# Kernel tuning notes

Measured on AMD Instinct MI355X. Metric: run time of the kernel, lower is better.

## Reference

```python
import jax, jax.numpy as jnp
import numpy as np

B = 32768          # batch
NA = 8             # n_agents
A = NA - 1         # other agents
OBS = 64
ACT = 14
OTH_IN = 82        # (sum(obs)+sum(act)-obs_i+act_i)//(NA-1)
H_SELF = 64
H_OTH = 128
H2 = 64
HEADS = 4
AD = H_OTH // HEADS  # 32
MAX_ACTION = 1.0
SCALE = float(np.sqrt(AD))


def setup_inputs() -> dict:
    key = jax.random.key(0)
    ks = jax.random.split(key, 24)
    r = jax.random.normal
    u = jax.random.uniform
    inp = {
        "state_one": r(ks[0], (B, OBS), jnp.float32),
        "act_one": u(ks[1], (B, ACT), jnp.float32),
        "state_others": r(ks[2], (A, B, OBS), jnp.float32),
        "act_others": u(ks[3], (A, B, OTH_IN - OBS), jnp.float32),
        # self encoder
        "W1": r(ks[4], (OBS + ACT, H_SELF), jnp.float32) * 0.05,
        "b1": r(ks[5], (H_SELF,), jnp.float32) * 0.05,
        "W2": r(ks[6], (H_SELF, H_SELF), jnp.float32) * 0.05,
        "b2": r(ks[7], (H_SELF,), jnp.float32) * 0.05,
        "w3_self": r(ks[8], (H_SELF, H2), jnp.float32) * 0.01,  # init.normal_(0, 0.01)
        # per-other-agent encoders (stacked ModuleList)
        "We": r(ks[9], (A, OTH_IN, H_OTH), jnp.float32) * 0.05,
        "be": r(ks[10], (A, H_OTH), jnp.float32) * 0.05,
        # attention heads (stacked)
        "Wk": r(ks[11], (HEADS, H_OTH, AD), jnp.float32) * 0.05,   # no bias
        "Wq": r(ks[12], (HEADS, H_SELF, AD), jnp.float32) * 0.05,  # no bias
        "Wv": r(ks[13], (HEADS, H_OTH, AD), jnp.float32) * 0.05,
        "bv": r(ks[14], (HEADS, AD), jnp.float32) * 0.05,
        "w3_others": r(ks[15], (H_OTH, H2), jnp.float32) * 0.01,
        "Wout": r(ks[16], (H2, 1), jnp.float32) * 0.05,
        "bout": r(ks[17], (1,), jnp.float32) * 0.05,
    }
    return inp


def reference(state_one, act_one, state_others, act_others,
              W1, b1, W2, b2, w3_self, We, be,
              Wk, Wq, Wv, bv, w3_others, Wout, bout):
    act_one = act_one / MAX_ACTION
    act_others = act_others / MAX_ACTION

    # self branch
    x = jnp.concatenate([state_one, act_one], axis=-1)          # [B, 78]
    x1 = jax.nn.relu(x @ W1 + b1)                               # [B, 64]
    x2 = jax.nn.relu(x1 @ W2 + b2)                              # [B, 64]
    x3_self = x2 @ w3_self                                      # [B, 64]

    # per-other-agent encoders
    inps = jnp.concatenate([state_others, act_others], axis=-1)  # [A, B, 82]
    enc = jax.nn.relu(jnp.einsum('abi,aij->abj', inps, We) + be[:, None, :])  # [A, B, 128]

    # multi-head attention: query from x1 (self), keys/values from encodings
    keys = jnp.einsum('abj,hjd->habd', enc, Wk)                  # [H, A, B, d]
    vals = jax.nn.relu(jnp.einsum('abj,hjd->habd', enc, Wv) + bv[:, None, None, :])
    sel = jnp.einsum('bj,hjd->hbd', x1, Wq)                      # [H, B, d]
    logits = jnp.einsum('hbd,habd->hba', sel, keys) / SCALE      # [H, B, A]
    w = jax.nn.softmax(logits, axis=-1)
    ov = jnp.einsum('habd,hba->hbd', vals, w)                    # [H, B, d]

    # concat heads along feature dim (head-major, as torch.cat over head list)
    x2_others = jnp.transpose(ov, (1, 0, 2)).reshape(-1, HEADS * AD)  # [B, 128]
    x3_others = x2_others @ w3_others                            # [B, 64]

    x3 = jax.nn.relu(x3_self + x3_others)
    return x3 @ Wout + bout                                      # [B, 1]
```

## Files before the change

kernel.cpp:

```cpp
#include <hip/hip_runtime.h>
#include <hip/hip_bf16.h>

#define BTOT 32768
#define TB 32

typedef __attribute__((ext_vector_type(8))) short bhalf8;
typedef __attribute__((ext_vector_type(4))) float f32x4;

static __device__ __forceinline__ unsigned short f2bf(float x) {
    __hip_bfloat16 h = __float2bfloat16(x);
    unsigned short u;
    __builtin_memcpy(&u, &h, sizeof(u));
    return u;
}
static __device__ __forceinline__ float bf2f(unsigned short s) {
    return __uint_as_float(((unsigned int)s) << 16);
}

__global__ __launch_bounds__(256) void prep_all(
        const float* __restrict__ Wk, const float* __restrict__ Wq,
        const float* __restrict__ We, const float* __restrict__ Wv,
        const float* __restrict__ W2, const float* __restrict__ w3_self,
        const float* __restrict__ w3_others, const float* __restrict__ W1,
        unsigned short* __restrict__ Mf2, unsigned short* __restrict__ Wef2,
        unsigned short* __restrict__ Wvf2, unsigned short* __restrict__ W2f,
        unsigned short* __restrict__ w3sf, unsigned short* __restrict__ w3of,
        unsigned short* __restrict__ W1f)
{
    const int blk = blockIdx.x;
    if (blk < 128) {
        int tid = blk * 256 + threadIdx.x;
        int h  = tid >> 13;
        int jq = (tid >> 7) & 63;
        int j  = tid & 127;
        const float* q = Wq + (h*64 + jq)*32;
        const float* k = Wk + (h*128 + j)*32;
        float acc = 0.f;
#pragma unroll
        for (int d = 0; d < 32; d += 4) {
            float4 a = *(const float4*)(q + d);
            float4 b = *(const float4*)(k + d);
            acc += a.x*b.x + a.y*b.y + a.z*b.z + a.w*b.w;
        }
        unsigned short hi = f2bf(acc);
        unsigned short lo = f2bf(acc - bf2f(hi));
        int n  = h*128 + j;
        int kt = jq >> 5, qd = (jq >> 3) & 3, jj = jq & 7;
        int nt = n >> 4,  ln = n & 15;
        size_t base = (((nt*2 + kt)*64) + qd*16 + ln)*16;
        Mf2[base + jj]     = hi;
        Mf2[base + 8 + jj] = lo;
    } else if (blk < 464) {
        int tid = (blk - 128) * 256 + threadIdx.x;
        int a = tid / 12288;
        int r = tid - a*12288;
        int k = r >> 7;
        int n = r & 127;
        float v = (k < 82) ? We[((size_t)a*82 + k)*128 + n] : 0.f;
        unsigned short hi = f2bf(v);
        unsigned short lo = f2bf(v - bf2f(hi));
        int kt = k >> 5, qd = (k >> 3) & 3, j = k & 7;
        int nt = n >> 4, ln = n & 15;
        size_t base = (size_t)a*24576 + (((nt*3 + kt)*64) + qd*16 + ln)*16;
        Wef2[base + j]     = hi;
        Wef2[base + 8 + j] = lo;
    } else if (blk < 528) {
        int tid = (blk - 464) * 256 + threadIdx.x;
        int h = tid >> 12;
        int j = (tid >> 5) & 127;
        int d = tid & 31;
        float v = Wv[tid];
        unsigned short hi = f2bf(v);
        unsigned short lo = f2bf(v - bf2f(hi));
        int k = j, n = h*32 + d;
        int kt = k >> 5, qd = (k >> 3) & 3, jj = k & 7;
        int nt = n >> 4, ln = n & 15;
        size_t base = (((nt*4 + kt)*64) + qd*16 + ln)*16;
        Wvf2[base + jj]     = hi;
        Wvf2[base + 8 + jj] = lo;
    } else {
        int tid = (blk - 528) * 256 + threadIdx.x;
        const float* src;
        unsigned short* dst;
        int idx, KT, kmax;
        if (tid < 4096)       { src = W2;        dst = W2f;  idx = tid;         KT = 2; kmax = 64; }
        else if (tid < 8192)  { src = w3_self;   dst = w3sf; idx = tid - 4096;  KT = 2; kmax = 64; }
        else if (tid < 16384) { src = w3_others; dst = w3of; idx = tid - 8192;  KT = 4; kmax = 128; }
        else                  { src = W1;        dst = W1f;  idx = tid - 16384; KT = 3; kmax = 78; }
        int k = idx >> 6;
        int n = idx & 63;
        float v = (k < kmax) ? src[k*64 + n] : 0.f;
        unsigned short hi = f2bf(v);
        unsigned short lo = f2bf(v - bf2f(hi));
        int kt = k >> 5, qd = (k >> 3) & 3, j = k & 7;
        int nt = n >> 4, ln = n & 15;
        size_t base = (((nt*KT + kt)*64) + qd*16 + ln)*16;
        dst[base + j]     = hi;
        dst[base + 8 + j] = lo;
    }
}

__global__ __launch_bounds__(256, 2) void fused_critic(
    const float* __restrict__ state_one, const float* __restrict__ act_one,
    const float* __restrict__ state_others, const float* __restrict__ act_others,
    const float* __restrict__ b1, const float* __restrict__ b2,
    const float* __restrict__ be, const float* __restrict__ bvp,
    const float* __restrict__ Wout, const float* __restrict__ bout,
    const unsigned short* __restrict__ Mf2, const unsigned short* __restrict__ Wef2,
    const unsigned short* __restrict__ Wvf2, const unsigned short* __restrict__ W2f,
    const unsigned short* __restrict__ w3sf, const unsigned short* __restrict__ w3of,
    const unsigned short* __restrict__ W1f, float* __restrict__ out)
{
    __shared__ __align__(16) unsigned char smem[33280];
    unsigned short* sXbH  = (unsigned short*)smem;
    unsigned short* sXbL  = (unsigned short*)(smem + 6656);
    unsigned short* sX1bH = (unsigned short*)(smem + 13312);
    unsigned short* sX1bL = (unsigned short*)(smem + 17920);
    unsigned short* sX2bH = (unsigned short*)(smem + 22528);
    unsigned short* sX2bL = (unsigned short*)(smem + 27136);
    unsigned short* sT    = (unsigned short*)smem;
    unsigned short* sInH  = (unsigned short*)smem;
    unsigned short* sInL  = (unsigned short*)(smem + 6656);
    unsigned short* sEnH  = (unsigned short*)(smem + 13312);
    unsigned short* sEnL  = (unsigned short*)(smem + 22016);
    unsigned short* sOvH  = (unsigned short*)smem;
    unsigned short* sOvL  = (unsigned short*)(smem + 8704);
    float*          sRed  = (float*)(smem + 17408);

    const int t  = threadIdx.x;
    const int b0 = blockIdx.x * TB;
    const int w  = t >> 6;
    const int l  = t & 63;
    const int m  = l & 15;
    const int qd = l >> 4;

    const int act_r = t >> 3, act_c = t & 7;

    auto stageIn = [&](const float4& vA, const float4& vB, const float* av) {
        const int r0 = t >> 4, c4 = (t & 15) << 2;
        ushort4 h4, l4;
        h4.x = f2bf(vA.x); l4.x = f2bf(vA.x - bf2f(h4.x));
        h4.y = f2bf(vA.y); l4.y = f2bf(vA.y - bf2f(h4.y));
        h4.z = f2bf(vA.z); l4.z = f2bf(vA.z - bf2f(h4.z));
        h4.w = f2bf(vA.w); l4.w = f2bf(vA.w - bf2f(h4.w));
        *(ushort4*)(sInH + r0*104 + c4) = h4;
        *(ushort4*)(sInL + r0*104 + c4) = l4;
        h4.x = f2bf(vB.x); l4.x = f2bf(vB.x - bf2f(h4.x));
        h4.y = f2bf(vB.y); l4.y = f2bf(vB.y - bf2f(h4.y));
        h4.z = f2bf(vB.z); l4.z = f2bf(vB.z - bf2f(h4.z));
        h4.w = f2bf(vB.w); l4.w = f2bf(vB.w - bf2f(h4.w));
        *(ushort4*)(sInH + (r0+16)*104 + c4) = h4;
        *(ushort4*)(sInL + (r0+16)*104 + c4) = l4;
        if (act_c < 6) {
#pragma unroll
            for (int e = 0; e < 3; ++e) {
                float v = av[e];
                unsigned short hh = f2bf(v);
                sInH[act_r*104 + 64 + act_c*3 + e] = hh;
                sInL[act_r*104 + 64 + act_c*3 + e] = f2bf(v - bf2f(hh));
            }
        }
    };

    {
        const int r0 = t >> 4, c4 = (t & 15) << 2;
        float4 vA = *(const float4*)(state_one + (size_t)(b0 + r0)*64 + c4);
        float4 vB = *(const float4*)(state_one + (size_t)(b0 + r0 + 16)*64 + c4);
        ushort4 h4, l4;
        h4.x = f2bf(vA.x); l4.x = f2bf(vA.x - bf2f(h4.x));
        h4.y = f2bf(vA.y); l4.y = f2bf(vA.y - bf2f(h4.y));
        h4.z = f2bf(vA.z); l4.z = f2bf(vA.z - bf2f(h4.z));
        h4.w = f2bf(vA.w); l4.w = f2bf(vA.w - bf2f(h4.w));
        *(ushort4*)(sXbH + r0*104 + c4) = h4;
        *(ushort4*)(sXbL + r0*104 + c4) = l4;
        h4.x = f2bf(vB.x); l4.x = f2bf(vB.x - bf2f(h4.x));
        h4.y = f2bf(vB.y); l4.y = f2bf(vB.y - bf2f(h4.y));
        h4.z = f2bf(vB.z); l4.z = f2bf(vB.z - bf2f(h4.z));
        h4.w = f2bf(vB.w); l4.w = f2bf(vB.w - bf2f(h4.w));
        *(ushort4*)(sXbH + (r0+16)*104 + c4) = h4;
        *(ushort4*)(sXbL + (r0+16)*104 + c4) = l4;
#pragma unroll
        for (int e = 0; e < 2; ++e) {
            int cc = act_c*2 + e;
            float v = (cc < 14) ? act_one[(size_t)(b0 + act_r)*14 + cc] : 0.f;
            unsigned short hh = f2bf(v);
            sXbH[act_r*104 + 64 + cc] = hh;
            sXbL[act_r*104 + 64 + cc] = f2bf(v - bf2f(hh));
        }
        for (int f = t; f < TB*16; f += 256) {
            int r = f >> 4, c = 80 + (f & 15);
            sXbH[r*104 + c] = 0;
            sXbL[r*104 + c] = 0;
        }
    }
    __syncthreads();

    {
        f32x4 acc1[2] = {};
#pragma unroll
        for (int kt = 0; kt < 3; ++kt) {
            bhalf8 ah0 = *(const bhalf8*)(sXbH + m*104      + kt*32 + qd*8);
            bhalf8 ah1 = *(const bhalf8*)(sXbH + (16+m)*104 + kt*32 + qd*8);
            bhalf8 al0 = *(const bhalf8*)(sXbL + m*104      + kt*32 + qd*8);
            bhalf8 al1 = *(const bhalf8*)(sXbL + (16+m)*104 + kt*32 + qd*8);
            const unsigned short* bp = W1f + ((w*3 + kt)*64 + l)*16;
            bhalf8 bh = *(const bhalf8*)(bp);
            bhalf8 bl = *(const bhalf8*)(bp + 8);
            acc1[0] = __builtin_amdgcn_mfma_f32_16x16x32_bf16(ah0, bh, acc1[0], 0, 0, 0);
            acc1[1] = __builtin_amdgcn_mfma_f32_16x16x32_bf16(ah1, bh, acc1[1], 0, 0, 0);
            acc1[0] = __builtin_amdgcn_mfma_f32_16x16x32_bf16(ah0, bl, acc1[0], 0, 0, 0);
            acc1[1] = __builtin_amdgcn_mfma_f32_16x16x32_bf16(ah1, bl, acc1[1], 0, 0, 0);
            acc1[0] = __builtin_amdgcn_mfma_f32_16x16x32_bf16(al0, bh, acc1[0], 0, 0, 0);
            acc1[1] = __builtin_amdgcn_mfma_f32_16x16x32_bf16(al1, bh, acc1[1], 0, 0, 0);
        }
        int col = w*16 + m;
        float b1c = b1[col];
#pragma unroll
        for (int rt = 0; rt < 2; ++rt)
#pragma unroll
            for (int r = 0; r < 4; ++r) {
                float e = fmaxf(acc1[rt][r] + b1c, 0.f);
                int row = rt*16 + qd*4 + r;
                unsigned short hh = f2bf(e);
                sX1bH[row*72 + col] = hh;
                sX1bL[row*72 + col] = f2bf(e - bf2f(hh));
            }
    }
    __syncthreads();

    {
        f32x4 acc2[2] = {};
#pragma unroll
        for (int kt = 0; kt < 2; ++kt) {
            bhalf8 ah0 = *(const bhalf8*)(sX1bH + m*72      + kt*32 + qd*8);
            bhalf8 ah1 = *(const bhalf8*)(sX1bH + (16+m)*72 + kt*32 + qd*8);
            bhalf8 al0 = *(const bhalf8*)(sX1bL + m*72      + kt*32 + qd*8);
            bhalf8 al1 = *(const bhalf8*)(sX1bL + (16+m)*72 + kt*32 + qd*8);
            const unsigned short* bp = W2f + ((w*2 + kt)*64 + l)*16;
            bhalf8 bh = *(const bhalf8*)(bp);
            bhalf8 bl = *(const bhalf8*)(bp + 8);
            acc2[0] = __builtin_amdgcn_mfma_f32_16x16x32_bf16(ah0, bh, acc2[0], 0, 0, 0);
            acc2[1] = __builtin_amdgcn_mfma_f32_16x16x32_bf16(ah1, bh, acc2[1], 0, 0, 0);
            acc2[0] = __builtin_amdgcn_mfma_f32_16x16x32_bf16(ah0, bl, acc2[0], 0, 0, 0);
            acc2[1] = __builtin_amdgcn_mfma_f32_16x16x32_bf16(ah1, bl, acc2[1], 0, 0, 0);
            acc2[0] = __builtin_amdgcn_mfma_f32_16x16x32_bf16(al0, bh, acc2[0], 0, 0, 0);
            acc2[1] = __builtin_amdgcn_mfma_f32_16x16x32_bf16(al1, bh, acc2[1], 0, 0, 0);
        }
        int col = w*16 + m;
        float b2c = b2[col];
#pragma unroll
        for (int rt = 0; rt < 2; ++rt)
#pragma unroll
            for (int r = 0; r < 4; ++r) {
                float e = fmaxf(acc2[rt][r] + b2c, 0.f);
                int row = rt*16 + qd*4 + r;
                unsigned short hh = f2bf(e);
                sX2bH[row*72 + col] = hh;
                sX2bL[row*72 + col] = f2bf(e - bf2f(hh));
            }
    }
    __syncthreads();

    f32x4 x3a[2] = {};
    {
#pragma unroll
        for (int kt = 0; kt < 2; ++kt) {
            bhalf8 ah0 = *(const bhalf8*)(sX2bH + m*72      + kt*32 + qd*8);
            bhalf8 ah1 = *(const bhalf8*)(sX2bH + (16+m)*72 + kt*32 + qd*8);
            bhalf8 al0 = *(const bhalf8*)(sX2bL + m*72      + kt*32 + qd*8);
            bhalf8 al1 = *(const bhalf8*)(sX2bL + (16+m)*72 + kt*32 + qd*8);
            const unsigned short* bp = w3sf + ((w*2 + kt)*64 + l)*16;
            bhalf8 bh = *(const bhalf8*)(bp);
            bhalf8 bl = *(const bhalf8*)(bp + 8);
            x3a[0] = __builtin_amdgcn_mfma_f32_16x16x32_bf16(ah0, bh, x3a[0], 0, 0, 0);
            x3a[1] = __builtin_amdgcn_mfma_f32_16x16x32_bf16(ah1, bh, x3a[1], 0, 0, 0);
            x3a[0] = __builtin_amdgcn_mfma_f32_16x16x32_bf16(ah0, bl, x3a[0], 0, 0, 0);
            x3a[1] = __builtin_amdgcn_mfma_f32_16x16x32_bf16(ah1, bl, x3a[1], 0, 0, 0);
            x3a[0] = __builtin_amdgcn_mfma_f32_16x16x32_bf16(al0, bh, x3a[0], 0, 0, 0);
            x3a[1] = __builtin_amdgcn_mfma_f32_16x16x32_bf16(al1, bh, x3a[1], 0, 0, 0);
        }
    }

    {
        f32x4 tacc[2][8] = {};
#pragma unroll
        for (int kt = 0; kt < 2; ++kt) {
            bhalf8 ah0 = *(const bhalf8*)(sX1bH + m*72      + kt*32 + qd*8);
            bhalf8 ah1 = *(const bhalf8*)(sX1bH + (16+m)*72 + kt*32 + qd*8);
            bhalf8 al0 = *(const bhalf8*)(sX1bL + m*72      + kt*32 + qd*8);
            bhalf8 al1 = *(const bhalf8*)(sX1bL + (16+m)*72 + kt*32 + qd*8);
#pragma unroll
            for (int nt2 = 0; nt2 < 8; ++nt2) {
                int nt = w*8 + nt2;
                const unsigned short* bp = Mf2 + ((nt*2 + kt)*64 + l)*16;
                bhalf8 bh = *(const bhalf8*)(bp);
                bhalf8 bl = *(const bhalf8*)(bp + 8);
                tacc[0][nt2] = __builtin_amdgcn_mfma_f32_16x16x32_bf16(ah0, bh, tacc[0][nt2], 0, 0, 0);
                tacc[1][nt2] = __builtin_amdgcn_mfma_f32_16x16x32_bf16(ah1, bh, tacc[1][nt2], 0, 0, 0);
                tacc[0][nt2] = __builtin_amdgcn_mfma_f32_16x16x32_bf16(ah0, bl, tacc[0][nt2], 0, 0, 0);
                tacc[1][nt2] = __builtin_amdgcn_mfma_f32_16x16x32_bf16(ah1, bl, tacc[1][nt2], 0, 0, 0);
                tacc[0][nt2] = __builtin_amdgcn_mfma_f32_16x16x32_bf16(al0, bh, tacc[0][nt2], 0, 0, 0);
                tacc[1][nt2] = __builtin_amdgcn_mfma_f32_16x16x32_bf16(al1, bh, tacc[1][nt2], 0, 0, 0);
            }
        }
        __syncthreads();
#pragma unroll
        for (int rt = 0; rt < 2; ++rt)
#pragma unroll
            for (int nt2 = 0; nt2 < 8; ++nt2)
#pragma unroll
                for (int r = 0; r < 4; ++r)
                    sT[(rt*16 + qd*4 + r)*520 + w*128 + nt2*16 + m] =
                        f2bf(tacc[rt][nt2][r]);
    }
    __syncthreads();

    bhalf8 tB0[4], tB1[4];
    {
#pragma unroll
        for (int kt = 0; kt < 4; ++kt) {
            tB0[kt] = *(const bhalf8*)(sT + m*520      + w*128 + kt*32 + qd*8);
            tB1[kt] = *(const bhalf8*)(sT + (16+m)*520 + w*128 + kt*32 + qd*8);
        }
    }
    __syncthreads();

    for (int f = t; f < TB*16; f += 256) {
        int r = f >> 4, c = f & 15;
        if (c >= 2) {
            sInH[r*104 + 80 + c] = 0;
            sInL[r*104 + 80 + c] = 0;
        }
    }
    {
        const float* sa = state_others + (size_t)b0 * 64;
        float4 vA = *(const float4*)(sa + t*4);
        float4 vB = *(const float4*)(sa + t*4 + 1024);
        float av[3] = {0.f, 0.f, 0.f};
        if (act_c < 6) {
            const float* aa = act_others + (size_t)(b0 + act_r)*18 + act_c*3;
            av[0] = aa[0]; av[1] = aa[1]; av[2] = aa[2];
        }
        stageIn(vA, vB, av);
    }
    __syncthreads();

    const float bv0 = bvp[w*32 + m];
    const float bv1 = bvp[w*32 + 16 + m];
    f32x4 o4[2][2] = {};
    float mR = -1e30f, sR = 0.f;

    const int nsel = l & 15;
    const int srcl = ((nsel >> 2) << 4) | nsel;

    float4 pfA, pfB; float pfa[3] = {0.f, 0.f, 0.f};

    for (int a = 0; a < 7; ++a) {
        if (a < 6) {
            const float* sa = state_others + ((size_t)(a+1)*BTOT + b0)*64;
            pfA = *(const float4*)(sa + t*4);
            pfB = *(const float4*)(sa + t*4 + 1024);
            if (act_c < 6) {
                const float* aa = act_others
                    + ((size_t)(a+1)*BTOT + b0 + act_r)*18 + act_c*3;
                pfa[0] = aa[0]; pfa[1] = aa[1]; pfa[2] = aa[2];
            }
        }
        float be0 = be[a*128 + 32*w + m];
        float be1 = be[a*128 + 32*w + 16 + m];

        f32x4 eacc[2][2] = {};
#pragma unroll
        for (int kt = 0; kt < 3; ++kt) {
            bhalf8 ah0 = *(const bhalf8*)(sInH + m*104      + kt*32 + qd*8);
            bhalf8 ah1 = *(const bhalf8*)(sInH + (16+m)*104 + kt*32 + qd*8);
            bhalf8 al0 = *(const bhalf8*)(sInL + m*104      + kt*32 + qd*8);
            bhalf8 al1 = *(const bhalf8*)(sInL + (16+m)*104 + kt*32 + qd*8);
#pragma unroll
            for (int nt2 = 0; nt2 < 2; ++nt2) {
                int nt = 2*w + nt2;
                const unsigned short* bp =
                    Wef2 + (size_t)a*24576 + ((nt*3 + kt)*64 + l)*16;
                bhalf8 bh = *(const bhalf8*)(bp);
                bhalf8 bl = *(const bhalf8*)(bp + 8);
                eacc[0][nt2] = __builtin_amdgcn_mfma_f32_16x16x32_bf16(ah0, bh, eacc[0][nt2], 0, 0, 0);
                eacc[1][nt2] = __builtin_amdgcn_mfma_f32_16x16x32_bf16(ah1, bh, eacc[1][nt2], 0, 0, 0);
                eacc[0][nt2] = __builtin_amdgcn_mfma_f32_16x16x32_bf16(ah0, bl, eacc[0][nt2], 0, 0, 0);
                eacc[1][nt2] = __builtin_amdgcn_mfma_f32_16x16x32_bf16(ah1, bl, eacc[1][nt2], 0, 0, 0);
                eacc[0][nt2] = __builtin_amdgcn_mfma_f32_16x16x32_bf16(al0, bh, eacc[0][nt2], 0, 0, 0);
                eacc[1][nt2] = __builtin_amdgcn_mfma_f32_16x16x32_bf16(al1, bh, eacc[1][nt2], 0, 0, 0);
            }
        }

        __syncthreads();

        {
#pragma unroll
            for (int rt = 0; rt < 2; ++rt)
#pragma unroll
                for (int nt2 = 0; nt2 < 2; ++nt2) {
                    float bb = nt2 ? be1 : be0;
#pragma unroll
                    for (int r = 0; r < 4; ++r) {
                        float e = fmaxf(eacc[rt][nt2][r] + bb, 0.f);
                        int row = rt*16 + qd*4 + r;
                        int col = 32*w + nt2*16 + m;
                        unsigned short hh = f2bf(e);
                        sEnH[row*136 + col] = hh;
                        sEnL[row*136 + col] = f2bf(e - bf2f(hh));
                    }
                }
        }
        if (a < 6) stageIn(pfA, pfB, pfa);

        __syncthreads();

        f32x4 vacc[2][2] = {};
        f32x4 lacc0 = {}, lacc1 = {};
#pragma unroll
        for (int kt = 0; kt < 4; ++kt) {
            bhalf8 ah0 = *(const bhalf8*)(sEnH + m*136      + kt*32 + qd*8);
            bhalf8 ah1 = *(const bhalf8*)(sEnH + (16+m)*136 + kt*32 + qd*8);
            bhalf8 al0 = *(const bhalf8*)(sEnL + m*136      + kt*32 + qd*8);
            bhalf8 al1 = *(const bhalf8*)(sEnL + (16+m)*136 + kt*32 + qd*8);
#pragma unroll
            for (int nt2 = 0; nt2 < 2; ++nt2) {
                int nt = 2*w + nt2;
                const unsigned short* bp = Wvf2 + ((nt*4 + kt)*64 + l)*16;
                bhalf8 bh = *(const bhalf8*)(bp);
                bhalf8 bl = *(const bhalf8*)(bp + 8);
                vacc[0][nt2] = __builtin_amdgcn_mfma_f32_16x16x32_bf16(ah0, bh, vacc[0][nt2], 0, 0, 0);
                vacc[1][nt2] = __builtin_amdgcn_mfma_f32_16x16x32_bf16(ah1, bh, vacc[1][nt2], 0, 0, 0);
                vacc[0][nt2] = __builtin_amdgcn_mfma_f32_16x16x32_bf16(ah0, bl, vacc[0][nt2], 0, 0, 0);
                vacc[1][nt2] = __builtin_amdgcn_mfma_f32_16x16x32_bf16(ah1, bl, vacc[1][nt2], 0, 0, 0);
                vacc[0][nt2] = __builtin_amdgcn_mfma_f32_16x16x32_bf16(al0, bh, vacc[0][nt2], 0, 0, 0);
                vacc[1][nt2] = __builtin_amdgcn_mfma_f32_16x16x32_bf16(al1, bh, vacc[1][nt2], 0, 0, 0);
            }
            lacc0 = __builtin_amdgcn_mfma_f32_16x16x32_bf16(ah0, tB0[kt], lacc0, 0, 0, 0);
            lacc0 = __builtin_amdgcn_mfma_f32_16x16x32_bf16(al0, tB0[kt], lacc0, 0, 0, 0);
            lacc1 = __builtin_amdgcn_mfma_f32_16x16x32_bf16(ah1, tB1[kt], lacc1, 0, 0, 0);
            lacc1 = __builtin_amdgcn_mfma_f32_16x16x32_bf16(al1, tB1[kt], lacc1, 0, 0, 0);
        }

        float alpha, pp;
        {
            float e01 = (l & 1) ? lacc0[1] : lacc0[0];
            float e23 = (l & 1) ? lacc0[3] : lacc0[2];
            float d0  = (l & 2) ? e23 : e01;
            float f01 = (l & 1) ? lacc1[1] : lacc1[0];
            float f23 = (l & 1) ? lacc1[3] : lacc1[2];
            float d1  = (l & 2) ? f23 : f01;
            float g0 = __shfl(d0, srcl);
            float g1 = __shfl(d1, srcl);
            float part = (l & 16) ? g1 : g0;
            float lg = part * 0.17677669529663687f;
            float mn = fmaxf(mR, lg);
            alpha = __expf(mR - mn);
            pp    = __expf(lg - mn);
            sR = sR*alpha + pp;
            mR = mn;
        }

        {
#pragma unroll
            for (int rt = 0; rt < 2; ++rt)
#pragma unroll
                for (int r = 0; r < 4; ++r) {
                    int row = rt*16 + qd*4 + r;
                    float al = __shfl(alpha, row);
                    float p  = __shfl(pp, row);
#pragma unroll
                    for (int nt2 = 0; nt2 < 2; ++nt2) {
                        float bb = nt2 ? bv1 : bv0;
                        o4[rt][nt2][r] = o4[rt][nt2][r]*al
                                       + p*fmaxf(vacc[rt][nt2][r] + bb, 0.f);
                    }
                }
        }
    }
    __syncthreads();

    {
        float rinv = 1.0f / sR;
#pragma unroll
        for (int rt = 0; rt < 2; ++rt)
#pragma unroll
            for (int r = 0; r < 4; ++r) {
                int row = rt*16 + qd*4 + r;
                float inv = __shfl(rinv, row);
#pragma unroll
                for (int nt2 = 0; nt2 < 2; ++nt2) {
                    float v = o4[rt][nt2][r]*inv;
                    int col = 32*w + nt2*16 + m;
                    unsigned short hh = f2bf(v);
                    sOvH[row*136 + col] = hh;
                    sOvL[row*136 + col] = f2bf(v - bf2f(hh));
                }
            }
    }
    __syncthreads();

    {
#pragma unroll
        for (int kt = 0; kt < 4; ++kt) {
            bhalf8 ah0 = *(const bhalf8*)(sOvH + m*136      + kt*32 + qd*8);
            bhalf8 ah1 = *(const bhalf8*)(sOvH + (16+m)*136 + kt*32 + qd*8);
            bhalf8 al0 = *(const bhalf8*)(sOvL + m*136      + kt*32 + qd*8);
            bhalf8 al1 = *(const bhalf8*)(sOvL + (16+m)*136 + kt*32 + qd*8);
            const unsigned short* bp = w3of + ((w*4 + kt)*64 + l)*16;
            bhalf8 bh = *(const bhalf8*)(bp);
            bhalf8 bl = *(const bhalf8*)(bp + 8);
            x3a[0] = __builtin_amdgcn_mfma_f32_16x16x32_bf16(ah0, bh, x3a[0], 0, 0, 0);
            x3a[1] = __builtin_amdgcn_mfma_f32_16x16x32_bf16(ah1, bh, x3a[1], 0, 0, 0);
            x3a[0] = __builtin_amdgcn_mfma_f32_16x16x32_bf16(ah0, bl, x3a[0], 0, 0, 0);
            x3a[1] = __builtin_amdgcn_mfma_f32_16x16x32_bf16(ah1, bl, x3a[1], 0, 0, 0);
            x3a[0] = __builtin_amdgcn_mfma_f32_16x16x32_bf16(al0, bh, x3a[0], 0, 0, 0);
            x3a[1] = __builtin_amdgcn_mfma_f32_16x16x32_bf16(al1, bh, x3a[1], 0, 0, 0);
        }
        float wo = Wout[w*16 + m];
#pragma unroll
        for (int rt = 0; rt < 2; ++rt)
#pragma unroll
            for (int r = 0; r < 4; ++r) {
                float p = fmaxf(x3a[rt][r], 0.f) * wo;
                p += __shfl_xor(p, 1);
                p += __shfl_xor(p, 2);
                p += __shfl_xor(p, 4);
                p += __shfl_xor(p, 8);
                if (m == 0)
                    sRed[(rt*16 + qd*4 + r)*4 + w] = p;
            }
    }
    __syncthreads();
    if (t < 32)
        out[b0 + t] = sRed[t*4+0] + sRed[t*4+1] + sRed[t*4+2] + sRed[t*4+3]
                    + bout[0];
}

extern "C" void kernel_launch(void* const* d_in, const int* in_sizes, int n_in,
                              void* d_out, int out_size, void* d_ws, size_t ws_size,
                              hipStream_t stream) {
    (void)in_sizes; (void)n_in; (void)out_size; (void)ws_size;
    const float* state_one    = (const float*)d_in[0];
    const float* act_one      = (const float*)d_in[1];
    const float* state_others = (const float*)d_in[2];
    const float* act_others   = (const float*)d_in[3];
    const float* W1           = (const float*)d_in[4];
    const float* b1           = (const float*)d_in[5];
    const float* W2           = (const float*)d_in[6];
    const float* b2           = (const float*)d_in[7];
    const float* w3_self      = (const float*)d_in[8];
    const float* We           = (const float*)d_in[9];
    const float* be           = (const float*)d_in[10];
    const float* Wk           = (const float*)d_in[11];
    const float* Wq           = (const float*)d_in[12];
    const float* Wv           = (const float*)d_in[13];
    const float* bv           = (const float*)d_in[14];
    const float* w3_others    = (const float*)d_in[15];
    const float* Wout         = (const float*)d_in[16];
    const float* bout         = (const float*)d_in[17];
    float* out = (float*)d_out;

    unsigned short* Mf2  = (unsigned short*)d_ws;
    unsigned short* Wef2 = (unsigned short*)((char*)d_ws + 131072);
    unsigned short* Wvf2 = (unsigned short*)((char*)d_ws + 475136);
    unsigned short* W2f  = (unsigned short*)((char*)d_ws + 540672);
    unsigned short* w3sf = (unsigned short*)((char*)d_ws + 557056);
    unsigned short* w3of = (unsigned short*)((char*)d_ws + 573440);
    unsigned short* W1f  = (unsigned short*)((char*)d_ws + 606208);

    prep_all<<<616, 256, 0, stream>>>(Wk, Wq, We, Wv, W2, w3_self, w3_others,
                                      W1, Mf2, Wef2, Wvf2, W2f, w3sf, w3of, W1f);
    fused_critic<<<BTOT/TB, 256, 0, stream>>>(
        state_one, act_one, state_others, act_others,
        b1, b2, be, bv, Wout, bout,
        Mf2, Wef2, Wvf2, W2f, w3sf, w3of, W1f, out);
}
```

Before: 201.9 us.

## Split 32-row batch tile across two 256-thread groups in 512-thread blocks

The fused critic kernel now launches 512 threads per block, and each group of four waves handles 16 of the block's 32 batch rows instead of one wave covering both 16-row tiles. This halves per-thread accumulator and register use and gives more waves to hide memory and MFMA latency. In exchange, each weight B-fragment loaded from global memory is reused for only one row tile, so weight traffic per block doubles, and the block barriers now synchronize twice as many waves.

```diff
diff --git a/kernel.cpp b/kernel.cpp
--- a/kernel.cpp
+++ b/kernel.cpp
@@ -100,7 +100,7 @@
     }
 }
 
-__global__ __launch_bounds__(256, 2) void fused_critic(
+__global__ __launch_bounds__(512) void fused_critic(
     const float* __restrict__ state_one, const float* __restrict__ act_one,
     const float* __restrict__ state_others, const float* __restrict__ act_others,
     const float* __restrict__ b1, const float* __restrict__ b2,
@@ -129,15 +129,16 @@
 
     const int t  = threadIdx.x;
     const int b0 = blockIdx.x * TB;
-    const int w  = t >> 6;
+    const int g  = t >> 8;
+    const int ro = g << 4;
+    const int w  = (t >> 6) & 3;
     const int l  = t & 63;
     const int m  = l & 15;
     const int qd = l >> 4;
 
-    const int act_r = t >> 3, act_c = t & 7;
-
-    auto stageIn = [&](const float4& vA, const float4& vB, const float* av) {
-        const int r0 = t >> 4, c4 = (t & 15) << 2;
+    const int r0 = t >> 4, c16 = t & 15, c4 = c16 << 2;
+
+    auto stageIn = [&](const float4& vA, float a0, float a1) {
         ushort4 h4, l4;
         h4.x = f2bf(vA.x); l4.x = f2bf(vA.x - bf2f(h4.x));
         h4.y = f2bf(vA.y); l4.y = f2bf(vA.y - bf2f(h4.y));
@@ -145,27 +146,18 @@
         h4.w = f2bf(vA.w); l4.w = f2bf(vA.w - bf2f(h4.w));
         *(ushort4*)(sInH + r0*104 + c4) = h4;
         *(ushort4*)(sInL + r0*104 + c4) = l4;
-        h4.x = f2bf(vB.x); l4.x = f2bf(vB.x - bf2f(h4.x));
-        h4.y = f2bf(vB.y); l4.y = f2bf(vB.y - bf2f(h4.y));
-        h4.z = f2bf(vB.z); l4.z = f2bf(vB.z - bf2f(h4.z));
-        h4.w = f2bf(vB.w); l4.w = f2bf(vB.w - bf2f(h4.w));
-        *(ushort4*)(sInH + (r0+16)*104 + c4) = h4;
-        *(ushort4*)(sInL + (r0+16)*104 + c4) = l4;
-        if (act_c < 6) {
-#pragma unroll
-            for (int e = 0; e < 3; ++e) {
-                float v = av[e];
-                unsigned short hh = f2bf(v);
-                sInH[act_r*104 + 64 + act_c*3 + e] = hh;
-                sInL[act_r*104 + 64 + act_c*3 + e] = f2bf(v - bf2f(hh));
-            }
+        unsigned short hh = f2bf(a0);
+        sInH[r0*104 + 64 + c16] = hh;
+        sInL[r0*104 + 64 + c16] = f2bf(a0 - bf2f(hh));
+        if (c16 < 2) {
+            unsigned short h2 = f2bf(a1);
+            sInH[r0*104 + 80 + c16] = h2;
+            sInL[r0*104 + 80 + c16] = f2bf(a1 - bf2f(h2));
         }
     };
 
     {
-        const int r0 = t >> 4, c4 = (t & 15) << 2;
         float4 vA = *(const float4*)(state_one + (size_t)(b0 + r0)*64 + c4);
-        float4 vB = *(const float4*)(state_one + (size_t)(b0 + r0 + 16)*64 + c4);
         ushort4 h4, l4;
         h4.x = f2bf(vA.x); l4.x = f2bf(vA.x - bf2f(h4.x));
         h4.y = f2bf(vA.y); l4.y = f2bf(vA.y - bf2f(h4.y));
@@ -173,209 +165,157 @@
         h4.w = f2bf(vA.w); l4.w = f2bf(vA.w - bf2f(h4.w));
         *(ushort4*)(sXbH + r0*104 + c4) = h4;
         *(ushort4*)(sXbL + r0*104 + c4) = l4;
-        h4.x = f2bf(vB.x); l4.x = f2bf(vB.x - bf2f(h4.x));
-        h4.y = f2bf(vB.y); l4.y = f2bf(vB.y - bf2f(h4.y));
-        h4.z = f2bf(vB.z); l4.z = f2bf(vB.z - bf2f(h4.z));
-        h4.w = f2bf(vB.w); l4.w = f2bf(vB.w - bf2f(h4.w));
-        *(ushort4*)(sXbH + (r0+16)*104 + c4) = h4;
-        *(ushort4*)(sXbL + (r0+16)*104 + c4) = l4;
-#pragma unroll
-        for (int e = 0; e < 2; ++e) {
-            int cc = act_c*2 + e;
-            float v = (cc < 14) ? act_one[(size_t)(b0 + act_r)*14 + cc] : 0.f;
-            unsigned short hh = f2bf(v);
-            sXbH[act_r*104 + 64 + cc] = hh;
-            sXbL[act_r*104 + 64 + cc] = f2bf(v - bf2f(hh));
-        }
-        for (int f = t; f < TB*16; f += 256) {
-            int r = f >> 4, c = 80 + (f & 15);
-            sXbH[r*104 + c] = 0;
-            sXbL[r*104 + c] = 0;
-        }
-    }
-    __syncthreads();
-
-    {
-        f32x4 acc1[2] = {};
+        float v = (c16 < 14) ? act_one[(size_t)(b0 + r0)*14 + c16] : 0.f;
+        unsigned short hh = f2bf(v);
+        sXbH[r0*104 + 64 + c16] = hh;
+        sXbL[r0*104 + 64 + c16] = f2bf(v - bf2f(hh));
+        sXbH[r0*104 + 80 + c16] = 0;
+        sXbL[r0*104 + 80 + c16] = 0;
+    }
+    __syncthreads();
+
+    {
+        f32x4 acc1 = {};
 #pragma unroll
         for (int kt = 0; kt < 3; ++kt) {
-            bhalf8 ah0 = *(const bhalf8*)(sXbH + m*104      + kt*32 + qd*8);
-            bhalf8 ah1 = *(const bhalf8*)(sXbH + (16+m)*104 + kt*32 + qd*8);
-            bhalf8 al0 = *(const bhalf8*)(sXbL + m*104      + kt*32 + qd*8);
-            bhalf8 al1 = *(const bhalf8*)(sXbL + (16+m)*104 + kt*32 + qd*8);
+            bhalf8 ah = *(const bhalf8*)(sXbH + (ro+m)*104 + kt*32 + qd*8);
+            bhalf8 al = *(const bhalf8*)(sXbL + (ro+m)*104 + kt*32 + qd*8);
             const unsigned short* bp = W1f + ((w*3 + kt)*64 + l)*16;
             bhalf8 bh = *(const bhalf8*)(bp);
             bhalf8 bl = *(const bhalf8*)(bp + 8);
-            acc1[0] = __builtin_amdgcn_mfma_f32_16x16x32_bf16(ah0, bh, acc1[0], 0, 0, 0);
-            acc1[1] = __builtin_amdgcn_mfma_f32_16x16x32_bf16(ah1, bh, acc1[1], 0, 0, 0);
-            acc1[0] = __builtin_amdgcn_mfma_f32_16x16x32_bf16(ah0, bl, acc1[0], 0, 0, 0);
-            acc1[1] = __builtin_amdgcn_mfma_f32_16x16x32_bf16(ah1, bl, acc1[1], 0, 0, 0);
-            acc1[0] = __builtin_amdgcn_mfma_f32_16x16x32_bf16(al0, bh, acc1[0], 0, 0, 0);
-            acc1[1] = __builtin_amdgcn_mfma_f32_16x16x32_bf16(al1, bh, acc1[1], 0, 0, 0);
+            acc1 = __builtin_amdgcn_mfma_f32_16x16x32_bf16(ah, bh, acc1, 0, 0, 0);
+            acc1 = __builtin_amdgcn_mfma_f32_16x16x32_bf16(ah, bl, acc1, 0, 0, 0);
+            acc1 = __builtin_amdgcn_mfma_f32_16x16x32_bf16(al, bh, acc1, 0, 0, 0);
         }
         int col = w*16 + m;
         float b1c = b1[col];
 #pragma unroll
-        for (int rt = 0; rt < 2; ++rt)
-#pragma unroll
-            for (int r = 0; r < 4; ++r) {
-                float e = fmaxf(acc1[rt][r] + b1c, 0.f);
-                int row = rt*16 + qd*4 + r;
-                unsigned short hh = f2bf(e);
-                sX1bH[row*72 + col] = hh;
-                sX1bL[row*72 + col] = f2bf(e - bf2f(hh));
-            }
-    }
-    __syncthreads();
-
-    {
-        f32x4 acc2[2] = {};
+        for (int r = 0; r < 4; ++r) {
+            float e = fmaxf(acc1[r] + b1c, 0.f);
+            int row = ro + qd*4 + r;
+            unsigned short hh = f2bf(e);
+            sX1bH[row*72 + col] = hh;
+            sX1bL[row*72 + col] = f2bf(e - bf2f(hh));
+        }
+    }
+    __syncthreads();
+
+    {
+        f32x4 acc2 = {};
 #pragma unroll
         for (int kt = 0; kt < 2; ++kt) {
-            bhalf8 ah0 = *(const bhalf8*)(sX1bH + m*72      + kt*32 + qd*8);
-            bhalf8 ah1 = *(const bhalf8*)(sX1bH + (16+m)*72 + kt*32 + qd*8);
-            bhalf8 al0 = *(const bhalf8*)(sX1bL + m*72      + kt*32 + qd*8);
-            bhalf8 al1 = *(const bhalf8*)(sX1bL + (16+m)*72 + kt*32 + qd*8);
+            bhalf8 ah = *(const bhalf8*)(sX1bH + (ro+m)*72 + kt*32 + qd*8);
+            bhalf8 al = *(const bhalf8*)(sX1bL + (ro+m)*72 + kt*32 + qd*8);
             const unsigned short* bp = W2f + ((w*2 + kt)*64 + l)*16;
             bhalf8 bh = *(const bhalf8*)(bp);
             bhalf8 bl = *(const bhalf8*)(bp + 8);
-            acc2[0] = __builtin_amdgcn_mfma_f32_16x16x32_bf16(ah0, bh, acc2[0], 0, 0, 0);
-            acc2[1] = __builtin_amdgcn_mfma_f32_16x16x32_bf16(ah1, bh, acc2[1], 0, 0, 0);
-            acc2[0] = __builtin_amdgcn_mfma_f32_16x16x32_bf16(ah0, bl, acc2[0], 0, 0, 0);
-            acc2[1] = __builtin_amdgcn_mfma_f32_16x16x32_bf16(ah1, bl, acc2[1], 0, 0, 0);
-            acc2[0] = __builtin_amdgcn_mfma_f32_16x16x32_bf16(al0, bh, acc2[0], 0, 0, 0);
-            acc2[1] = __builtin_amdgcn_mfma_f32_16x16x32_bf16(al1, bh, acc2[1], 0, 0, 0);
+            acc2 = __builtin_amdgcn_mfma_f32_16x16x32_bf16(ah, bh, acc2, 0, 0, 0);
+            acc2 = __builtin_amdgcn_mfma_f32_16x16x32_bf16(ah, bl, acc2, 0, 0, 0);
+            acc2 = __builtin_amdgcn_mfma_f32_16x16x32_bf16(al, bh, acc2, 0, 0, 0);
         }
         int col = w*16 + m;
         float b2c = b2[col];
 #pragma unroll
-        for (int rt = 0; rt < 2; ++rt)
-#pragma unroll
-            for (int r = 0; r < 4; ++r) {
-                float e = fmaxf(acc2[rt][r] + b2c, 0.f);
-                int row = rt*16 + qd*4 + r;
-                unsigned short hh = f2bf(e);
-                sX2bH[row*72 + col] = hh;
-                sX2bL[row*72 + col] = f2bf(e - bf2f(hh));
-            }
-    }
-    __syncthreads();
-
-    f32x4 x3a[2] = {};
+        for (int r = 0; r < 4; ++r) {
+            float e = fmaxf(acc2[r] + b2c, 0.f);
+            int row = ro + qd*4 + r;
+            unsigned short hh = f2bf(e);
+            sX2bH[row*72 + col] = hh;
+            sX2bL[row*72 + col] = f2bf(e - bf2f(hh));
+        }
+    }
+    __syncthreads();
+
+    f32x4 x3a = {};
     {
 #pragma unroll
         for (int kt = 0; kt < 2; ++kt) {
-            bhalf8 ah0 = *(const bhalf8*)(sX2bH + m*72      + kt*32 + qd*8);
-            bhalf8 ah1 = *(const bhalf8*)(sX2bH + (16+m)*72 + kt*32 + qd*8);
-            bhalf8 al0 = *(const bhalf8*)(sX2bL + m*72      + kt*32 + qd*8);
-            bhalf8 al1 = *(const bhalf8*)(sX2bL + (16+m)*72 + kt*32 + qd*8);
+            bhalf8 ah = *(const bhalf8*)(sX2bH + (ro+m)*72 + kt*32 + qd*8);
+            bhalf8 al = *(const bhalf8*)(sX2bL + (ro+m)*72 + kt*32 + qd*8);
             const unsigned short* bp = w3sf + ((w*2 + kt)*64 + l)*16;
             bhalf8 bh = *(const bhalf8*)(bp);
             bhalf8 bl = *(const bhalf8*)(bp + 8);
-            x3a[0] = __builtin_amdgcn_mfma_f32_16x16x32_bf16(ah0, bh, x3a[0], 0, 0, 0);
-            x3a[1] = __builtin_amdgcn_mfma_f32_16x16x32_bf16(ah1, bh, x3a[1], 0, 0, 0);
-            x3a[0] = __builtin_amdgcn_mfma_f32_16x16x32_bf16(ah0, bl, x3a[0], 0, 0, 0);
-            x3a[1] = __builtin_amdgcn_mfma_f32_16x16x32_bf16(ah1, bl, x3a[1], 0, 0, 0);
-            x3a[0] = __builtin_amdgcn_mfma_f32_16x16x32_bf16(al0, bh, x3a[0], 0, 0, 0);
-            x3a[1] = __builtin_amdgcn_mfma_f32_16x16x32_bf16(al1, bh, x3a[1], 0, 0, 0);
-        }
-    }
-
-    {
-        f32x4 tacc[2][8] = {};
+            x3a = __builtin_amdgcn_mfma_f32_16x16x32_bf16(ah, bh, x3a, 0, 0, 0);
+            x3a = __builtin_amdgcn_mfma_f32_16x16x32_bf16(ah, bl, x3a, 0, 0, 0);
+            x3a = __builtin_amdgcn_mfma_f32_16x16x32_bf16(al, bh, x3a, 0, 0, 0);
+        }
+    }
+
+    {
+        f32x4 tacc[8] = {};
 #pragma unroll
         for (int kt = 0; kt < 2; ++kt) {
-            bhalf8 ah0 = *(const bhalf8*)(sX1bH + m*72      + kt*32 + qd*8);
-            bhalf8 ah1 = *(const bhalf8*)(sX1bH + (16+m)*72 + kt*32 + qd*8);
-            bhalf8 al0 = *(const bhalf8*)(sX1bL + m*72      + kt*32 + qd*8);
-            bhalf8 al1 = *(const bhalf8*)(sX1bL + (16+m)*72 + kt*32 + qd*8);
+            bhalf8 ah = *(const bhalf8*)(sX1bH + (ro+m)*72 + kt*32 + qd*8);
+            bhalf8 al = *(const bhalf8*)(sX1bL + (ro+m)*72 + kt*32 + qd*8);
 #pragma unroll
             for (int nt2 = 0; nt2 < 8; ++nt2) {
                 int nt = w*8 + nt2;
                 const unsigned short* bp = Mf2 + ((nt*2 + kt)*64 + l)*16;
                 bhalf8 bh = *(const bhalf8*)(bp);
                 bhalf8 bl = *(const bhalf8*)(bp + 8);
-                tacc[0][nt2] = __builtin_amdgcn_mfma_f32_16x16x32_bf16(ah0, bh, tacc[0][nt2], 0, 0, 0);
-                tacc[1][nt2] = __builtin_amdgcn_mfma_f32_16x16x32_bf16(ah1, bh, tacc[1][nt2], 0, 0, 0);
-                tacc[0][nt2] = __builtin_amdgcn_mfma_f32_16x16x32_bf16(ah0, bl, tacc[0][nt2], 0, 0, 0);
-                tacc[1][nt2] = __builtin_amdgcn_mfma_f32_16x16x32_bf16(ah1, bl, tacc[1][nt2], 0, 0, 0);
-                tacc[0][nt2] = __builtin_amdgcn_mfma_f32_16x16x32_bf16(al0, bh, tacc[0][nt2], 0, 0, 0);
-                tacc[1][nt2] = __builtin_amdgcn_mfma_f32_16x16x32_bf16(al1, bh, tacc[1][nt2], 0, 0, 0);
+                tacc[nt2] = __builtin_amdgcn_mfma_f32_16x16x32_bf16(ah, bh, tacc[nt2], 0, 0, 0);
+                tacc[nt2] = __builtin_amdgcn_mfma_f32_16x16x32_bf16(ah, bl, tacc[nt2], 0, 0, 0);
+                tacc[nt2] = __builtin_amdgcn_mfma_f32_16x16x32_bf16(al, bh, tacc[nt2], 0, 0, 0);
             }
         }
         __syncthreads();
 #pragma unroll
-        for (int rt = 0; rt < 2; ++rt)
-#pragma unroll
-            for (int nt2 = 0; nt2 < 8; ++nt2)
-#pragma unroll
-                for (int r = 0; r < 4; ++r)
-                    sT[(rt*16 + qd*4 + r)*520 + w*128 + nt2*16 + m] =
-                        f2bf(tacc[rt][nt2][r]);
-    }
-    __syncthreads();
-
-    bhalf8 tB0[4], tB1[4];
-    {
-#pragma unroll
-        for (int kt = 0; kt < 4; ++kt) {
-            tB0[kt] = *(const bhalf8*)(sT + m*520      + w*128 + kt*32 + qd*8);
-            tB1[kt] = *(const bhalf8*)(sT + (16+m)*520 + w*128 + kt*32 + qd*8);
-        }
-    }
-    __syncthreads();
-
-    for (int f = t; f < TB*16; f += 256) {
-        int r = f >> 4, c = f & 15;
-        if (c >= 2) {
-            sInH[r*104 + 80 + c] = 0;
-            sInL[r*104 + 80 + c] = 0;
-        }
+        for (int nt2 = 0; nt2 < 8; ++nt2)
+#pragma unroll
+            for (int r = 0; r < 4; ++r)
+                sT[(ro + qd*4 + r)*520 + w*128 + nt2*16 + m] =
+                    f2bf(tacc[nt2][r]);
+    }
+    __syncthreads();
+
+    bhalf8 tB0[4];
+    {
+#pragma unroll
+        for (int kt = 0; kt < 4; ++kt)
+            tB0[kt] = *(const bhalf8*)(sT + (ro+m)*520 + w*128 + kt*32 + qd*8);
+    }
+    __syncthreads();
+
+    if (c16 >= 2) {
+        sInH[r0*104 + 80 + c16] = 0;
+        sInL[r0*104 + 80 + c16] = 0;
     }
     {
         const float* sa = state_others + (size_t)b0 * 64;
         float4 vA = *(const float4*)(sa + t*4);
-        float4 vB = *(const float4*)(sa + t*4 + 1024);
-        float av[3] = {0.f, 0.f, 0.f};
-        if (act_c < 6) {
-            const float* aa = act_others + (size_t)(b0 + act_r)*18 + act_c*3;
-            av[0] = aa[0]; av[1] = aa[1]; av[2] = aa[2];
-        }
-        stageIn(vA, vB, av);
+        const float* aa = act_others + (size_t)(b0 + r0)*18;
+        float a0 = aa[c16];
+        float a1 = (c16 < 2) ? aa[16 + c16] : 0.f;
+        stageIn(vA, a0, a1);
     }
     __syncthreads();
 
     const float bv0 = bvp[w*32 + m];
     const float bv1 = bvp[w*32 + 16 + m];
-    f32x4 o4[2][2] = {};
+    f32x4 o4[2] = {};
     float mR = -1e30f, sR = 0.f;
 
     const int nsel = l & 15;
     const int srcl = ((nsel >> 2) << 4) | nsel;
 
-    float4 pfA, pfB; float pfa[3] = {0.f, 0.f, 0.f};
+    float4 pfA; float pa0 = 0.f, pa1 = 0.f;
 
     for (int a = 0; a < 7; ++a) {
         if (a < 6) {
             const float* sa = state_others + ((size_t)(a+1)*BTOT + b0)*64;
             pfA = *(const float4*)(sa + t*4);
-            pfB = *(const float4*)(sa + t*4 + 1024);
-            if (act_c < 6) {
-                const float* aa = act_others
-                    + ((size_t)(a+1)*BTOT + b0 + act_r)*18 + act_c*3;
-                pfa[0] = aa[0]; pfa[1] = aa[1]; pfa[2] = aa[2];
-            }
+            const float* aa = act_others + ((size_t)(a+1)*BTOT + b0 + r0)*18;
+            pa0 = aa[c16];
+            pa1 = (c16 < 2) ? aa[16 + c16] : 0.f;
         }
         float be0 = be[a*128 + 32*w + m];
         float be1 = be[a*128 + 32*w + 16 + m];
 
-        f32x4 eacc[2][2] = {};
+        f32x4 eacc[2] = {};
 #pragma unroll
         for (int kt = 0; kt < 3; ++kt) {
-            bhalf8 ah0 = *(const bhalf8*)(sInH + m*104      + kt*32 + qd*8);
-            bhalf8 ah1 = *(const bhalf8*)(sInH + (16+m)*104 + kt*32 + qd*8);
-            bhalf8 al0 = *(const bhalf8*)(sInL + m*104      + kt*32 + qd*8);
-            bhalf8 al1 = *(const bhalf8*)(sInL + (16+m)*104 + kt*32 + qd*8);
+            bhalf8 ah = *(const bhalf8*)(sInH + (ro+m)*104 + kt*32 + qd*8);
+            bhalf8 al = *(const bhalf8*)(sInL + (ro+m)*104 + kt*32 + qd*8);
 #pragma unroll
             for (int nt2 = 0; nt2 < 2; ++nt2) {
                 int nt = 2*w + nt2;
@@ -383,12 +323,9 @@
                     Wef2 + (size_t)a*24576 + ((nt*3 + kt)*64 + l)*16;
                 bhalf8 bh = *(const bhalf8*)(bp);
                 bhalf8 bl = *(const bhalf8*)(bp + 8);
-                eacc[0][nt2] = __builtin_amdgcn_mfma_f32_16x16x32_bf16(ah0, bh, eacc[0][nt2], 0, 0, 0);
-                eacc[1][nt2] = __builtin_amdgcn_mfma_f32_16x16x32_bf16(ah1, bh, eacc[1][nt2], 0, 0, 0);
-                eacc[0][nt2] = __builtin_amdgcn_mfma_f32_16x16x32_bf16(ah0, bl, eacc[0][nt2], 0, 0, 0);
-                eacc[1][nt2] = __builtin_amdgcn_mfma_f32_16x16x32_bf16(ah1, bl, eacc[1][nt2], 0, 0, 0);
-                eacc[0][nt2] = __builtin_amdgcn_mfma_f32_16x16x32_bf16(al0, bh, eacc[0][nt2], 0, 0, 0);
-                eacc[1][nt2] = __builtin_amdgcn_mfma_f32_16x16x32_bf16(al1, bh, eacc[1][nt2], 0, 0, 0);
+                eacc[nt2] = __builtin_amdgcn_mfma_f32_16x16x32_bf16(ah, bh, eacc[nt2], 0, 0, 0);
+                eacc[nt2] = __builtin_amdgcn_mfma_f32_16x16x32_bf16(ah, bl, eacc[nt2], 0, 0, 0);
+                eacc[nt2] = __builtin_amdgcn_mfma_f32_16x16x32_bf16(al, bh, eacc[nt2], 0, 0, 0);
             }
         }
 
@@ -396,64 +333,50 @@
 
         {
 #pragma unroll
-            for (int rt = 0; rt < 2; ++rt)
-#pragma unroll
-                for (int nt2 = 0; nt2 < 2; ++nt2) {
-                    float bb = nt2 ? be1 : be0;
-#pragma unroll
-                    for (int r = 0; r < 4; ++r) {
-                        float e = fmaxf(eacc[rt][nt2][r] + bb, 0.f);
-                        int row = rt*16 + qd*4 + r;
-                        int col = 32*w + nt2*16 + m;
-                        unsigned short hh = f2bf(e);
-                        sEnH[row*136 + col] = hh;
-                        sEnL[row*136 + col] = f2bf(e - bf2f(hh));
-                    }
+            for (int nt2 = 0; nt2 < 2; ++nt2) {
+                float bb = nt2 ? be1 : be0;
+#pragma unroll
+                for (int r = 0; r < 4; ++r) {
+                    float e = fmaxf(eacc[nt2][r] + bb, 0.f);
+                    int row = ro + qd*4 + r;
+                    int col = 32*w + nt2*16 + m;
+                    unsigned short hh = f2bf(e);
+                    sEnH[row*136 + col] = hh;
+                    sEnL[row*136 + col] = f2bf(e - bf2f(hh));
                 }
-        }
-        if (a < 6) stageIn(pfA, pfB, pfa);
+            }
+        }
+        if (a < 6) stageIn(pfA, pa0, pa1);
 
         __syncthreads();
 
-        f32x4 vacc[2][2] = {};
-        f32x4 lacc0 = {}, lacc1 = {};
+        f32x4 vacc[2] = {};
+        f32x4 lacc = {};
 #pragma unroll
         for (int kt = 0; kt < 4; ++kt) {
-            bhalf8 ah0 = *(const bhalf8*)(sEnH + m*136      + kt*32 + qd*8);
-            bhalf8 ah1 = *(const bhalf8*)(sEnH + (16+m)*136 + kt*32 + qd*8);
-            bhalf8 al0 = *(const bhalf8*)(sEnL + m*136      + kt*32 + qd*8);
-            bhalf8 al1 = *(const bhalf8*)(sEnL + (16+m)*136 + kt*32 + qd*8);
+            bhalf8 ah = *(const bhalf8*)(sEnH + (ro+m)*136 + kt*32 + qd*8);
+            bhalf8 al = *(const bhalf8*)(sEnL + (ro+m)*136 + kt*32 + qd*8);
 #pragma unroll
             for (int nt2 = 0; nt2 < 2; ++nt2) {
                 int nt = 2*w + nt2;
                 const unsigned short* bp = Wvf2 + ((nt*4 + kt)*64 + l)*16;
                 bhalf8 bh = *(const bhalf8*)(bp);
                 bhalf8 bl = *(const bhalf8*)(bp + 8);
-                vacc[0][nt2] = __builtin_amdgcn_mfma_f32_16x16x32_bf16(ah0, bh, vacc[0][nt2], 0, 0, 0);
-                vacc[1][nt2] = __builtin_amdgcn_mfma_f32_16x16x32_bf16(ah1, bh, vacc[1][nt2], 0, 0, 0);
-                vacc[0][nt2] = __builtin_amdgcn_mfma_f32_16x16x32_bf16(ah0, bl, vacc[0][nt2], 0, 0, 0);
-                vacc[1][nt2] = __builtin_amdgcn_mfma_f32_16x16x32_bf16(ah1, bl, vacc[1][nt2], 0, 0, 0);
-                vacc[0][nt2] = __builtin_amdgcn_mfma_f32_16x16x32_bf16(al0, bh, vacc[0][nt2], 0, 0, 0);
-                vacc[1][nt2] = __builtin_amdgcn_mfma_f32_16x16x32_bf16(al1, bh, vacc[1][nt2], 0, 0, 0);
-            }
-            lacc0 = __builtin_amdgcn_mfma_f32_16x16x32_bf16(ah0, tB0[kt], lacc0, 0, 0, 0);
-            lacc0 = __builtin_amdgcn_mfma_f32_16x16x32_bf16(al0, tB0[kt], lacc0, 0, 0, 0);
-            lacc1 = __builtin_amdgcn_mfma_f32_16x16x32_bf16(ah1, tB1[kt], lacc1, 0, 0, 0);
-            lacc1 = __builtin_amdgcn_mfma_f32_16x16x32_bf16(al1, tB1[kt], lacc1, 0, 0, 0);
+                vacc[nt2] = __builtin_amdgcn_mfma_f32_16x16x32_bf16(ah, bh, vacc[nt2], 0, 0, 0);
+                vacc[nt2] = __builtin_amdgcn_mfma_f32_16x16x32_bf16(ah, bl, vacc[nt2], 0, 0, 0);
+                vacc[nt2] = __builtin_amdgcn_mfma_f32_16x16x32_bf16(al, bh, vacc[nt2], 0, 0, 0);
+            }
+            lacc = __builtin_amdgcn_mfma_f32_16x16x32_bf16(ah, tB0[kt], lacc, 0, 0, 0);
+            lacc = __builtin_amdgcn_mfma_f32_16x16x32_bf16(al, tB0[kt], lacc, 0, 0, 0);
         }
 
         float alpha, pp;
         {
-            float e01 = (l & 1) ? lacc0[1] : lacc0[0];
-            float e23 = (l & 1) ? lacc0[3] : lacc0[2];
+            float e01 = (l & 1) ? lacc[1] : lacc[0];
+            float e23 = (l & 1) ? lacc[3] : lacc[2];
             float d0  = (l & 2) ? e23 : e01;
-            float f01 = (l & 1) ? lacc1[1] : lacc1[0];
-            float f23 = (l & 1) ? lacc1[3] : lacc1[2];
-            float d1  = (l & 2) ? f23 : f01;
-            float g0 = __shfl(d0, srcl);
-            float g1 = __shfl(d1, srcl);
-            float part = (l & 16) ? g1 : g0;
-            float lg = part * 0.17677669529663687f;
+            float g0  = __shfl(d0, srcl);
+            float lg  = g0 * 0.17677669529663687f;
             float mn = fmaxf(mR, lg);
             alpha = __expf(mR - mn);
             pp    = __expf(lg - mn);
@@ -463,19 +386,17 @@
 
         {
 #pragma unroll
-            for (int rt = 0; rt < 2; ++rt)
-#pragma unroll
-                for (int r = 0; r < 4; ++r) {
-                    int row = rt*16 + qd*4 + r;
-                    float al = __shfl(alpha, row);
-                    float p  = __shfl(pp, row);
-#pragma unroll
-                    for (int nt2 = 0; nt2 < 2; ++nt2) {
-                        float bb = nt2 ? bv1 : bv0;
-                        o4[rt][nt2][r] = o4[rt][nt2][r]*al
-                                       + p*fmaxf(vacc[rt][nt2][r] + bb, 0.f);
-                    }
+            for (int r = 0; r < 4; ++r) {
+                int row = qd*4 + r;
+                float al_ = __shfl(alpha, row);
+                float p   = __shfl(pp, row);
+#pragma unroll
+                for (int nt2 = 0; nt2 < 2; ++nt2) {
+                    float bb = nt2 ? bv1 : bv0;
+                    o4[nt2][r] = o4[nt2][r]*al_
+                               + p*fmaxf(vacc[nt2][r] + bb, 0.f);
                 }
+            }
         }
     }
     __syncthreads();
@@ -483,53 +404,44 @@
     {
         float rinv = 1.0f / sR;
 #pragma unroll
-        for (int rt = 0; rt < 2; ++rt)
-#pragma unroll
-            for (int r = 0; r < 4; ++r) {
-                int row = rt*16 + qd*4 + r;
-                float inv = __shfl(rinv, row);
-#pragma unroll
-                for (int nt2 = 0; nt2 < 2; ++nt2) {
-                    float v = o4[rt][nt2][r]*inv;
-                    int col = 32*w + nt2*16 + m;
-                    unsigned short hh = f2bf(v);
-                    sOvH[row*136 + col] = hh;
-                    sOvL[row*136 + col] = f2bf(v - bf2f(hh));
-                }
-            }
+        for (int r = 0; r < 4; ++r) {
+            float inv = __shfl(rinv, qd*4 + r);
+            int row = ro + qd*4 + r;
+#pragma unroll
+            for (int nt2 = 0; nt2 < 2; ++nt2) {
+                float v = o4[nt2][r]*inv;
+                int col = 32*w + nt2*16 + m;
+                unsigned short hh = f2bf(v);
+                sOvH[row*136 + col] = hh;
+                sOvL[row*136 + col] = f2bf(v - bf2f(hh));
+            }
+        }
     }
     __syncthreads();
 
     {
 #pragma unroll
         for (int kt = 0; kt < 4; ++kt) {
-            bhalf8 ah0 = *(const bhalf8*)(sOvH + m*136      + kt*32 + qd*8);
-            bhalf8 ah1 = *(const bhalf8*)(sOvH + (16+m)*136 + kt*32 + qd*8);
-            bhalf8 al0 = *(const bhalf8*)(sOvL + m*136      + kt*32 + qd*8);
-            bhalf8 al1 = *(const bhalf8*)(sOvL + (16+m)*136 + kt*32 + qd*8);
+            bhalf8 ah = *(const bhalf8*)(sOvH + (ro+m)*136 + kt*32 + qd*8);
+            bhalf8 al = *(const bhalf8*)(sOvL + (ro+m)*136 + kt*32 + qd*8);
             const unsigned short* bp = w3of + ((w*4 + kt)*64 + l)*16;
             bhalf8 bh = *(const bhalf8*)(bp);
             bhalf8 bl = *(const bhalf8*)(bp + 8);
-            x3a[0] = __builtin_amdgcn_mfma_f32_16x16x32_bf16(ah0, bh, x3a[0], 0, 0, 0);
-            x3a[1] = __builtin_amdgcn_mfma_f32_16x16x32_bf16(ah1, bh, x3a[1], 0, 0, 0);
-            x3a[0] = __builtin_amdgcn_mfma_f32_16x16x32_bf16(ah0, bl, x3a[0], 0, 0, 0);
-            x3a[1] = __builtin_amdgcn_mfma_f32_16x16x32_bf16(ah1, bl, x3a[1], 0, 0, 0);
-            x3a[0] = __builtin_amdgcn_mfma_f32_16x16x32_bf16(al0, bh, x3a[0], 0, 0, 0);
-            x3a[1] = __builtin_amdgcn_mfma_f32_16x16x32_bf16(al1, bh, x3a[1], 0, 0, 0);
+            x3a = __builtin_amdgcn_mfma_f32_16x16x32_bf16(ah, bh, x3a, 0, 0, 0);
+            x3a = __builtin_amdgcn_mfma_f32_16x16x32_bf16(ah, bl, x3a, 0, 0, 0);
+            x3a = __builtin_amdgcn_mfma_f32_16x16x32_bf16(al, bh, x3a, 0, 0, 0);
         }
         float wo = Wout[w*16 + m];
 #pragma unroll
-        for (int rt = 0; rt < 2; ++rt)
-#pragma unroll
-            for (int r = 0; r < 4; ++r) {
-                float p = fmaxf(x3a[rt][r], 0.f) * wo;
-                p += __shfl_xor(p, 1);
-                p += __shfl_xor(p, 2);
-                p += __shfl_xor(p, 4);
-                p += __shfl_xor(p, 8);
-                if (m == 0)
-                    sRed[(rt*16 + qd*4 + r)*4 + w] = p;
-            }
+        for (int r = 0; r < 4; ++r) {
+            float p = fmaxf(x3a[r], 0.f) * wo;
+            p += __shfl_xor(p, 1);
+            p += __shfl_xor(p, 2);
+            p += __shfl_xor(p, 4);
+            p += __shfl_xor(p, 8);
+            if (m == 0)
+                sRed[(ro + qd*4 + r)*4 + w] = p;
+        }
     }
     __syncthreads();
     if (t < 32)
@@ -571,7 +483,7 @@
 
     prep_all<<<616, 256, 0, stream>>>(Wk, Wq, We, Wv, W2, w3_self, w3_others,
                                       W1, Mf2, Wef2, Wvf2, W2f, w3sf, w3of, W1f);
-    fused_critic<<<BTOT/TB, 256, 0, stream>>>(
+    fused_critic<<<BTOT/TB, 512, 0, stream>>>(
         state_one, act_one, state_others, act_others,
         b1, b2, be, bv, Wout, bout,
         Mf2, Wef2, Wvf2, W2f, w3sf, w3of, W1f, out);
```

Measured after the change: 233.4 us. 1.16x slower.
